# Kernel optimization log

Measured on AMD Instinct MI355X. Metric: run time of the kernel, lower is better.

Reference implementation:

```python
import jax, jax.numpy as jnp
import numpy as np

N, E, G, H, C = 50000, 800000, 512, 4, 64
DIN, DENC = 128, 256


def setup_inputs() -> dict:
    key = jax.random.key(0)
    ks = jax.random.split(key, 12)
    inp = {
        "hy": jax.random.normal(ks[0], (1, G, DENC), jnp.float32),
        "x": jax.random.normal(ks[1], (N, DIN), jnp.float32),
        "edge_index": jax.random.randint(ks[2], (2, E), 0, N, jnp.int32),
        "batch": jnp.sort(jax.random.randint(ks[3], (N,), 0, G, jnp.int32)),
        # GATv2Conv params (lin_l, lin_r: DIN -> H*C; att: [H, C]; bias: [C] since concat=False)
        "Wl": jax.random.normal(ks[4], (DIN, H * C), jnp.float32) * (1.0 / np.sqrt(DIN)),
        "bl": jnp.zeros((H * C,), jnp.float32),
        "Wr": jax.random.normal(ks[5], (DIN, H * C), jnp.float32) * (1.0 / np.sqrt(DIN)),
        "br": jnp.zeros((H * C,), jnp.float32),
        "att": jax.random.normal(ks[6], (H, C), jnp.float32) * (1.0 / np.sqrt(C)),
        "bias_gnn": jnp.zeros((C,), jnp.float32),
        # fc: (DENC + 64) -> DENC
        "Wfc": jax.random.normal(ks[7], (DENC + C, DENC), jnp.float32) * (1.0 / np.sqrt(DENC + C)),
        "bfc": jnp.zeros((DENC,), jnp.float32),
    }
    return inp


def _gatv2(x, edge_index, Wl, bl, Wr, br, att, bias_gnn):
    # add self loops (PyG default)
    loops = jnp.arange(N, dtype=edge_index.dtype)
    src = jnp.concatenate([edge_index[0], loops])
    dst = jnp.concatenate([edge_index[1], loops])
    xl = (x @ Wl + bl).reshape(N, H, C)  # source transform
    xr = (x @ Wr + br).reshape(N, H, C)  # target transform
    s = jax.nn.leaky_relu(xl[src] + xr[dst], 0.2)        # [Et, H, C]
    e = jnp.einsum('ehc,hc->eh', s, att)                 # [Et, H]
    # segment softmax over incoming edges of each dst node
    m = jax.ops.segment_max(e, dst, num_segments=N)
    m = jnp.where(jnp.isfinite(m), m, 0.0)
    a = jnp.exp(e - m[dst])
    denom = jax.ops.segment_sum(a, dst, num_segments=N)
    alpha = a / (denom[dst] + 1e-16)                     # [Et, H]
    msg = xl[src] * alpha[:, :, None]                    # [Et, H, C]
    out = jax.ops.segment_sum(msg, dst, num_segments=N)  # [N, H, C]
    return out.mean(axis=1) + bias_gnn                   # concat=False -> head mean


def reference(hy, x, edge_index, batch, Wl, bl, Wr, br, att, bias_gnn, Wfc, bfc):
    h = jax.nn.leaky_relu(_gatv2(x, edge_index, Wl, bl, Wr, br, att, bias_gnn), 0.01)
    # global mean pool per graph
    sums = jax.ops.segment_sum(h, batch, num_segments=G)
    cnts = jax.ops.segment_sum(jnp.ones((N, 1), h.dtype), batch, num_segments=G)
    hg = (sums / jnp.maximum(cnts, 1.0))[None]           # [1, G, C]
    cat = jnp.concatenate([hy, hg], axis=2)              # [1, G, DENC+C]
    return cat @ Wfc + bfc
```

## Files before the change

kernel.cpp:

```cpp
#include <hip/hip_runtime.h>

typedef unsigned short u16;
typedef __attribute__((ext_vector_type(8))) short bf16x8;
typedef __attribute__((ext_vector_type(4))) float f32x4;
typedef __attribute__((ext_vector_type(2))) float f32x2;

constexpr int N    = 50000;
constexpr int E    = 800000;
constexpr int G    = 512;
constexpr int HC   = 256;
constexpr int DIN  = 128;
constexpr int DENC = 256;
constexpr int DFC  = 320;
constexpr int NBLK = (N + 1023) / 1024;
constexpr int MT   = 64;
constexpr int XB   = (N + MT - 1) / MT;

__device__ __forceinline__ float bf2f(u16 u) {
    return __uint_as_float(((unsigned)u) << 16);
}
__device__ __forceinline__ u16 f2bf(float f) {
    unsigned u = __float_as_uint(f);
    u += 0x7fffu + ((u >> 16) & 1u);
    return (u16)(u >> 16);
}
__device__ __forceinline__ float lrelu(float v, float s) {
    return v > 0.0f ? v : v * s;
}

template<int CTRL>
__device__ __forceinline__ float dpp_radd(float x) {
    int y = __builtin_amdgcn_update_dpp(0, __float_as_int(x), CTRL, 0xF, 0xF, true);
    return x + __int_as_float(y);
}

template<bool BF> __device__ __forceinline__ float ld(const void* p, size_t i) {
    if constexpr (BF) return bf2f(((const u16*)p)[i]);
    else              return ((const float*)p)[i];
}
template<bool BF> __device__ __forceinline__ float4 ld4(const void* p, size_t i) {
    if constexpr (BF) {
        ushort4 v = ((const ushort4*)p)[i >> 2];
        return make_float4(bf2f(v.x), bf2f(v.y), bf2f(v.z), bf2f(v.w));
    } else {
        return ((const float4*)p)[i >> 2];
    }
}
template<bool BF> __device__ __forceinline__ void st(void* p, size_t i, float v) {
    if constexpr (BF) ((u16*)p)[i] = f2bf(v);
    else              ((float*)p)[i] = v;
}
__device__ __forceinline__ float ldr(const void* p, size_t i, bool bf) {
    return bf ? bf2f(((const u16*)p)[i]) : ((const float*)p)[i];
}

__global__ void k_detect(const void* x, int* flag) {
    if (blockIdx.x == 0 && threadIdx.x == 0) {
        const u16* p = (const u16*)x;
        int ok = 0;
        for (int i = 0; i < 256; i++) {
            unsigned e = (p[i] >> 7) & 0xffu;
            if (e == 0u || (e >= 100u && e <= 140u)) ok++;
        }
        *flag = (ok >= 218) ? 0 : 1;
    }
}

__global__ __launch_bounds__(64) void k_wprep(const void* Wl, const void* Wr,
                                              u16* __restrict__ whi, u16* __restrict__ wlo,
                                              const int* __restrict__ flag) {
    bool bf = (*flag == 0);
    int tile = blockIdx.x;
    int l = threadIdx.x;
    int c = tile & 31, s = tile >> 5;
    int col = c * 16 + (l & 15);
    int kbase = s * 32 + ((l >> 4) * 8);
    size_t o = (size_t)tile * 512 + (size_t)l * 8;
    #pragma unroll
    for (int j = 0; j < 8; j++) {
        int k = kbase + j;
        float v = (col < HC) ? ldr(Wl, (size_t)k * HC + col, bf)
                             : ldr(Wr, (size_t)k * HC + (col - HC), bf);
        u16 h = f2bf(v);
        whi[o + j] = h;
        wlo[o + j] = f2bf(v - bf2f(h));
    }
}

template<bool BF>
__global__ __launch_bounds__(256) void k_xlxr_t(
    const void* __restrict__ x, const u16* __restrict__ whi, const u16* __restrict__ wlo,
    const void* __restrict__ bl, const void* __restrict__ br,
    u16* __restrict__ xl, u16* __restrict__ xr, const int* __restrict__ flag) {
    if ((*flag == 0) != BF) return;
    __shared__ u16 ah[MT][136];
    __shared__ u16 al[BF ? 1 : MT][136];
    int b = blockIdx.x, t = threadIdx.x;
    int row0 = b * MT;

    {
        int k0 = (t & 15) * 8;
        #pragma unroll
        for (int it = 0; it < 4; it++) {
            int r = (t >> 4) + it * 16;
            int g = row0 + r; if (g >= N) g = N - 1;
            size_t base = (size_t)g * DIN + k0;
            if constexpr (BF) {
                const ushort4* xp = (const ushort4*)x;
                *(ushort4*)&ah[r][k0]     = xp[base >> 2];
                *(ushort4*)&ah[r][k0 + 4] = xp[(base >> 2) + 1];
            } else {
                const float4* xp = (const float4*)x;
                float4 f0 = xp[base >> 2], f1 = xp[(base >> 2) + 1];
                float v[8] = {f0.x, f0.y, f0.z, f0.w, f1.x, f1.y, f1.z, f1.w};
                #pragma unroll
                for (int j = 0; j < 8; j++) {
                    u16 h = f2bf(v[j]);
                    ah[r][k0 + j] = h;
                    al[r][k0 + j] = f2bf(v[j] - bf2f(h));
                }
            }
        }
    }
    __syncthreads();

    int w = t >> 6, l = t & 63;
    int rl = l & 15, kg = (l >> 4) * 8;
    f32x4 acc[4][8];
    #pragma unroll
    for (int rt = 0; rt < 4; rt++)
        #pragma unroll
        for (int ci = 0; ci < 8; ci++) {
            f32x4 z = {0.f, 0.f, 0.f, 0.f};
            acc[rt][ci] = z;
        }

    #pragma unroll
    for (int s = 0; s < 4; s++) {
        bf16x8 a0 = *(const bf16x8*)&ah[rl][s * 32 + kg];
        bf16x8 a1 = *(const bf16x8*)&ah[16 + rl][s * 32 + kg];
        bf16x8 a2 = *(const bf16x8*)&ah[32 + rl][s * 32 + kg];
        bf16x8 a3 = *(const bf16x8*)&ah[48 + rl][s * 32 + kg];
        #pragma unroll
        for (int ci = 0; ci < 8; ci++) {
            int c = w * 8 + ci;
            size_t fo = ((size_t)(s * 32 + c) * 64 + l) * 8;
            bf16x8 bh = *(const bf16x8*)&whi[fo];
            acc[0][ci] = __builtin_amdgcn_mfma_f32_16x16x32_bf16(a0, bh, acc[0][ci], 0, 0, 0);
            acc[1][ci] = __builtin_amdgcn_mfma_f32_16x16x32_bf16(a1, bh, acc[1][ci], 0, 0, 0);
            acc[2][ci] = __builtin_amdgcn_mfma_f32_16x16x32_bf16(a2, bh, acc[2][ci], 0, 0, 0);
            acc[3][ci] = __builtin_amdgcn_mfma_f32_16x16x32_bf16(a3, bh, acc[3][ci], 0, 0, 0);
            if constexpr (!BF) {
                bf16x8 e0 = *(const bf16x8*)&al[rl][s * 32 + kg];
                bf16x8 e1 = *(const bf16x8*)&al[16 + rl][s * 32 + kg];
                bf16x8 e2 = *(const bf16x8*)&al[32 + rl][s * 32 + kg];
                bf16x8 e3 = *(const bf16x8*)&al[48 + rl][s * 32 + kg];
                bf16x8 bw = *(const bf16x8*)&wlo[fo];
                acc[0][ci] = __builtin_amdgcn_mfma_f32_16x16x32_bf16(a0, bw, acc[0][ci], 0, 0, 0);
                acc[0][ci] = __builtin_amdgcn_mfma_f32_16x16x32_bf16(e0, bh, acc[0][ci], 0, 0, 0);
                acc[1][ci] = __builtin_amdgcn_mfma_f32_16x16x32_bf16(a1, bw, acc[1][ci], 0, 0, 0);
                acc[1][ci] = __builtin_amdgcn_mfma_f32_16x16x32_bf16(e1, bh, acc[1][ci], 0, 0, 0);
                acc[2][ci] = __builtin_amdgcn_mfma_f32_16x16x32_bf16(a2, bw, acc[2][ci], 0, 0, 0);
                acc[2][ci] = __builtin_amdgcn_mfma_f32_16x16x32_bf16(e2, bh, acc[2][ci], 0, 0, 0);
                acc[3][ci] = __builtin_amdgcn_mfma_f32_16x16x32_bf16(a3, bw, acc[3][ci], 0, 0, 0);
                acc[3][ci] = __builtin_amdgcn_mfma_f32_16x16x32_bf16(e3, bh, acc[3][ci], 0, 0, 0);
            }
        }
    }
    __syncthreads();

    float fbias[8];
    #pragma unroll
    for (int ci = 0; ci < 8; ci++) {
        int col = (w * 8 + ci) * 16 + (l & 15);
        fbias[ci] = (col < HC) ? ld<BF>(bl, col) : ld<BF>(br, col - HC);
    }

    u16 (*ep)[520] = reinterpret_cast<u16 (*)[520]>(&ah[0][0]);
    int r4 = (l >> 4) * 4;
    #pragma unroll
    for (int rt = 0; rt < 4; rt++) {
        #pragma unroll
        for (int ci = 0; ci < 8; ci++) {
            int col = (w * 8 + ci) * 16 + (l & 15);
            #pragma unroll
            for (int i = 0; i < 4; i++)
                ep[r4 + i][col] = f2bf(acc[rt][ci][i] + fbias[ci]);
        }
        __syncthreads();
        #pragma unroll
        for (int j = 0; j < 4; j++) {
            int q   = t + 256 * j;
            int row = q >> 6;
            int ck  = q & 63;
            int gr  = row0 + rt * 16 + row;
            uint4 v = *(const uint4*)&ep[row][ck * 8];
            int col0 = ck * 8;
            if (gr < N) {
                u16* dst = (col0 < HC) ? xl : xr;
                int  cc  = col0 & (HC - 1);
                *(uint4*)&dst[(size_t)gr * HC + cc] = v;
            }
        }
        __syncthreads();
    }
}

__global__ void k_deg(const int* __restrict__ ei, int* __restrict__ deg) {
    int e = blockIdx.x * blockDim.x + threadIdx.x;
    if (e < E) {
        int d = ei[E + e];
        if ((unsigned)d < (unsigned)N) atomicAdd(&deg[d], 1);
    }
}

__global__ void k_chunksum(const int* __restrict__ deg, int* __restrict__ blocksum) {
    int b = blockIdx.x, t = threadIdx.x;
    int base = b * 1024 + t * 4;
    int s = 0;
    #pragma unroll
    for (int i = 0; i < 4; i++) { int idx = base + i; if (idx < N) s += deg[idx]; }
    for (int off = 32; off; off >>= 1) s += __shfl_down(s, off, 64);
    __shared__ int ls[4];
    int wave = t >> 6;
    if ((t & 63) == 0) ls[wave] = s;
    __syncthreads();
    if (t == 0) blocksum[b] = ls[0] + ls[1] + ls[2] + ls[3];
}

__global__ void k_scanoff(int* __restrict__ blocksum, int* __restrict__ rowptr) {
    if (threadIdx.x == 0 && blockIdx.x == 0) {
        int run = 0;
        for (int b = 0; b < NBLK; b++) { int v = blocksum[b]; blocksum[b] = run; run += v; }
        rowptr[N] = run;
    }
}

__global__ void k_scanwrite(const int* __restrict__ deg, const int* __restrict__ blocksum,
                            int* __restrict__ rowptr) {
    int b = blockIdx.x, t = threadIdx.x;
    int base = b * 1024 + t * 4;
    int v[4]; int s = 0;
    #pragma unroll
    for (int i = 0; i < 4; i++) { v[i] = (base + i < N) ? deg[base + i] : 0; s += v[i]; }
    int lane = t & 63, wave = t >> 6;
    int x = s;
    for (int off = 1; off < 64; off <<= 1) {
        int y = __shfl_up(x, off, 64);
        if (lane >= off) x += y;
    }
    __shared__ int wtot[4];
    if (lane == 63) wtot[wave] = x;
    __syncthreads();
    int woff = 0;
    for (int w = 0; w < wave; w++) woff += wtot[w];
    int run = blocksum[b] + woff + (x - s);
    #pragma unroll
    for (int i = 0; i < 4; i++) {
        int idx = base + i;
        if (idx < N) rowptr[idx] = run;
        run += v[i];
    }
}

__global__ void k_fill(const int* __restrict__ ei, const int* __restrict__ rowptr,
                       int* __restrict__ cursor, int* __restrict__ col) {
    int e = blockIdx.x * blockDim.x + threadIdx.x;
    if (e < E) {
        int d = ei[E + e];
        if ((unsigned)d < (unsigned)N) {
            int pos = atomicAdd(&cursor[d], 1);
            unsigned idx = (unsigned)(rowptr[d] + pos);
            int s = ei[e];
            if (idx < (unsigned)E) col[idx] = ((unsigned)s < (unsigned)N) ? s : d;
        }
    }
}

template<bool BF>
__device__ void gat_body(const u16* __restrict__ xl, const u16* __restrict__ xr,
                         const int* __restrict__ rowptr, const int* __restrict__ col,
                         const void* __restrict__ att, const void* __restrict__ bias_gnn,
                         float* __restrict__ hnode) {
    int wid = (blockIdx.x * blockDim.x + threadIdx.x) >> 6;
    int lane = threadIdx.x & 63;
    if (wid >= N) return;
    int node = wid;

    const char* xlb = (const char*)xl;
    unsigned loff = (unsigned)lane << 3;
    auto loadrow = [&](int src) -> uint2 {
        return *(const uint2*)(xlb + (((unsigned)src << 9) + loff));
    };

    uint2 xrv = *(const uint2*)(((const char*)xr) + (((unsigned)node << 9) + loff));
    f32x2 ra, rb;
    ra.x = __uint_as_float(xrv.x << 16);
    ra.y = __uint_as_float(xrv.x & 0xffff0000u);
    rb.x = __uint_as_float(xrv.y << 16);
    rb.y = __uint_as_float(xrv.y & 0xffff0000u);
    float4 atv = ld4<BF>(att, (size_t)lane * 4);
    f32x2 ta = {atv.x, atv.y}, tb = {atv.z, atv.w};

    float l = 0.f;
    f32x2 aa = {0.f, 0.f}, ab = {0.f, 0.f};

    auto edge = [&](uint2 xv) {
        f32x2 xa, xb;
        xa.x = __uint_as_float(xv.x << 16);
        xa.y = __uint_as_float(xv.x & 0xffff0000u);
        xb.x = __uint_as_float(xv.y << 16);
        xb.y = __uint_as_float(xv.y & 0xffff0000u);
        f32x2 ua = xa + ra, ub = xb + rb;
        f32x2 sa = __builtin_elementwise_max(ua * 0.2f, ua);
        f32x2 sb = __builtin_elementwise_max(ub * 0.2f, ub);
        f32x2 d  = sa * ta + sb * tb;
        float p = d.x + d.y;
        p = dpp_radd<0xB1>(p);
        p = dpp_radd<0x4E>(p);
        p = dpp_radd<0x141>(p);
        p = dpp_radd<0x140>(p);
        float wgt = __expf(fminf(p, 80.0f));
        l += wgt;
        f32x2 wv = {wgt, wgt};
        aa = aa + xa * wv;
        ab = ab + xb * wv;
    };

    edge(loadrow(node));

    int beg = rowptr[node], end = rowptr[node + 1];
    beg = max(0, min(beg, E));
    end = max(beg, min(end, E));
    beg = __builtin_amdgcn_readfirstlane(beg);
    end = __builtin_amdgcn_readfirstlane(end);

    constexpr int UNR = 8;
    int j = beg;
    for (; j + UNR <= end; j += UNR) {
        int srcs[UNR];
        #pragma unroll
        for (int u = 0; u < UNR; u++) srcs[u] = col[j + u];
        uint2 vv[UNR];
        #pragma unroll
        for (int u = 0; u < UNR; u++) vv[u] = loadrow(srcs[u]);
        #pragma unroll
        for (int u = 0; u < UNR; u++) edge(vv[u]);
    }
    for (; j < end; j++) edge(loadrow(col[j]));

    float inv = 1.0f / (l + 1e-16f);
    float a0 = aa.x * inv, a1 = aa.y * inv, a2 = ab.x * inv, a3 = ab.y * inv;
    a0 += __shfl_xor(a0, 16); a0 += __shfl_xor(a0, 32);
    a1 += __shfl_xor(a1, 16); a1 += __shfl_xor(a1, 32);
    a2 += __shfl_xor(a2, 16); a2 += __shfl_xor(a2, 32);
    a3 += __shfl_xor(a3, 16); a3 += __shfl_xor(a3, 32);
    if (lane < 16) {
        float4 bv = ld4<BF>(bias_gnn, (size_t)lane * 4);
        float4 o;
        o.x = lrelu(a0 * 0.25f + bv.x, 0.01f);
        o.y = lrelu(a1 * 0.25f + bv.y, 0.01f);
        o.z = lrelu(a2 * 0.25f + bv.z, 0.01f);
        o.w = lrelu(a3 * 0.25f + bv.w, 0.01f);
        reinterpret_cast<float4*>(hnode)[(size_t)node * 16 + lane] = o;
    }
}

__global__ __launch_bounds__(256, 8) void k_gat(
    const u16* xl, const u16* xr, const int* rowptr, const int* col,
    const void* att, const void* bias_gnn, float* hnode, const int* flag) {
    if (*flag == 0) gat_body<true>(xl, xr, rowptr, col, att, bias_gnn, hnode);
    else            gat_body<false>(xl, xr, rowptr, col, att, bias_gnn, hnode);
}

__global__ __launch_bounds__(256) void k_pool(const float* __restrict__ hnode,
                                              const int* __restrict__ batch,
                                              float* __restrict__ hg) {
    int g = blockIdx.x, t = threadIdx.x;
    int lane = t & 63, w = t >> 6;
    int lo = 0, hi = N;
    while (lo < hi) { int mid = (lo + hi) >> 1; if (batch[mid] < g) lo = mid + 1; else hi = mid; }
    int s0 = lo;
    hi = N;
    while (lo < hi) { int mid = (lo + hi) >> 1; if (batch[mid] < g + 1) lo = mid + 1; else hi = mid; }
    int s1 = lo;
    float sum = 0.f;
    for (int n = s0 + w; n < s1; n += 4) sum += hnode[(size_t)n * 64 + lane];
    __shared__ float red[4][64];
    red[w][lane] = sum;
    __syncthreads();
    if (w == 0) {
        float s = red[0][lane] + red[1][lane] + red[2][lane] + red[3][lane];
        int cnt = s1 - s0; if (cnt < 1) cnt = 1;
        hg[g * 64 + lane] = s / (float)cnt;
    }
}

template<bool BF>
__device__ void fc_body(const void* __restrict__ hy, const float* __restrict__ hg,
                        const void* __restrict__ Wfc, const void* __restrict__ bfc,
                        void* __restrict__ out) {
    int g = blockIdx.x, t = threadIdx.x;
    __shared__ float cat[DFC];
    cat[t] = ld<BF>(hy, (size_t)g * DENC + t);
    if (t < 64) cat[DENC + t] = hg[g * 64 + t];
    __syncthreads();
    float acc = ld<BF>(bfc, t);
    for (int k = 0; k < DFC; k++) acc = fmaf(cat[k], ld<BF>(Wfc, (size_t)k * DENC + t), acc);
    st<BF>(out, (size_t)g * DENC + t, acc);
}

__global__ __launch_bounds__(256) void k_fc(
    const void* hy, const float* hg, const void* Wfc, const void* bfc,
    void* out, const int* flag) {
    if (*flag == 0) fc_body<true>(hy, hg, Wfc, bfc, out);
    else            fc_body<false>(hy, hg, Wfc, bfc, out);
}

extern "C" void kernel_launch(void* const* d_in, const int* in_sizes, int n_in,
                              void* d_out, int out_size, void* d_ws, size_t ws_size,
                              hipStream_t stream) {
    const void* hy   = d_in[0];
    const void* x    = d_in[1];
    const int*  ei   = (const int*)d_in[2];
    const int*  batch= (const int*)d_in[3];
    const void* Wl   = d_in[4];
    const void* bl   = d_in[5];
    const void* Wr   = d_in[6];
    const void* br   = d_in[7];
    const void* att  = d_in[8];
    const void* bias = d_in[9];
    const void* Wfc  = d_in[10];
    const void* bfc  = d_in[11];

    char* w = (char*)d_ws;
    u16*  xl      = (u16*)w;   w += (size_t)N * HC * 2;
    u16*  xr      = (u16*)w;   w += (size_t)N * HC * 2;
    float* hnode  = (float*)w; w += (size_t)N * 64 * 4;
    float* hg     = (float*)w; w += (size_t)G * 64 * 4;
    int*  col     = (int*)w;   w += (size_t)E * 4;
    int*  rowptr  = (int*)w;   w += ((size_t)N + 16) * 4;
    int*  blocksum= (int*)w;   w += 64 * 4;
    int*  flag    = (int*)w;   w += 64 * 4;
    int*  deg     = (int*)w;   w += (size_t)N * 4;
    int*  cursor  = (int*)w;   w += (size_t)N * 4;
    u16*  whi     = (u16*)w;   w += (size_t)4 * 32 * 64 * 8 * 2;
    u16*  wlo     = (u16*)w;   w += (size_t)4 * 32 * 64 * 8 * 2;

    hipMemsetAsync(deg, 0, (size_t)2 * N * 4, stream);

    k_detect<<<1, 64, 0, stream>>>(x, flag);
    k_wprep<<<128, 64, 0, stream>>>(Wl, Wr, whi, wlo, flag);
    k_xlxr_t<true ><<<XB, 256, 0, stream>>>(x, whi, wlo, bl, br, xl, xr, flag);
    k_xlxr_t<false><<<XB, 256, 0, stream>>>(x, whi, wlo, bl, br, xl, xr, flag);
    k_deg<<<(E + 255) / 256, 256, 0, stream>>>(ei, deg);
    k_chunksum<<<NBLK, 256, 0, stream>>>(deg, blocksum);
    k_scanoff<<<1, 64, 0, stream>>>(blocksum, rowptr);
    k_scanwrite<<<NBLK, 256, 0, stream>>>(deg, blocksum, rowptr);
    k_fill<<<(E + 255) / 256, 256, 0, stream>>>(ei, rowptr, cursor, col);
    k_gat<<<(N * 64 + 255) / 256, 256, 0, stream>>>(xl, xr, rowptr, col, att, bias, hnode, flag);
    k_pool<<<G, 256, 0, stream>>>(hnode, batch, hg);
    k_fc<<<G, 256, 0, stream>>>(hy, hg, Wfc, bfc, d_out, flag);
}
```

Measured before the change: 320.9 us.

## Split xl/xr GEMM blocks by output half to cut registers and raise occupancy

The projection kernel now launches twice as many blocks, each computing either the xl or the xr half of the 512 output columns for a 64-row tile. This halves the accumulator array per thread and merges the hi/lo LDS buffers, with launch bounds requesting four blocks per CU, so more waves can hide latency. The cost is that every x tile is loaded and split into bf16 hi/lo twice, once per column half, and the epilogue is simplified to write into a single destination.

```diff
diff --git a/kernel.cpp b/kernel.cpp
--- a/kernel.cpp
+++ b/kernel.cpp
@@ -15,6 +15,7 @@
 constexpr int NBLK = (N + 1023) / 1024;
 constexpr int MT   = 64;
 constexpr int XB   = (N + MT - 1) / MT;
+constexpr int CBLK = 4;
 
 __device__ __forceinline__ float bf2f(u16 u) {
     return __uint_as_float(((unsigned)u) << 16);
@@ -88,15 +89,15 @@
 }
 
 template<bool BF>
-__global__ __launch_bounds__(256) void k_xlxr_t(
+__global__ __launch_bounds__(256, 4) void k_xlxr_t(
     const void* __restrict__ x, const u16* __restrict__ whi, const u16* __restrict__ wlo,
     const void* __restrict__ bl, const void* __restrict__ br,
     u16* __restrict__ xl, u16* __restrict__ xr, const int* __restrict__ flag) {
     if ((*flag == 0) != BF) return;
-    __shared__ u16 ah[MT][136];
-    __shared__ u16 al[BF ? 1 : MT][136];
+    __shared__ u16 ah[(BF ? 1 : 2) * MT][136];
     int b = blockIdx.x, t = threadIdx.x;
-    int row0 = b * MT;
+    int rb = b >> 1, cg = b & 1;
+    int row0 = rb * MT;
 
     {
         int k0 = (t & 15) * 8;
@@ -117,7 +118,7 @@
                 for (int j = 0; j < 8; j++) {
                     u16 h = f2bf(v[j]);
                     ah[r][k0 + j] = h;
-                    al[r][k0 + j] = f2bf(v[j] - bf2f(h));
+                    ah[MT + r][k0 + j] = f2bf(v[j] - bf2f(h));
                 }
             }
         }
@@ -126,11 +127,11 @@
 
     int w = t >> 6, l = t & 63;
     int rl = l & 15, kg = (l >> 4) * 8;
-    f32x4 acc[4][8];
+    f32x4 acc[4][CBLK];
     #pragma unroll
     for (int rt = 0; rt < 4; rt++)
         #pragma unroll
-        for (int ci = 0; ci < 8; ci++) {
+        for (int ci = 0; ci < CBLK; ci++) {
             f32x4 z = {0.f, 0.f, 0.f, 0.f};
             acc[rt][ci] = z;
         }
@@ -142,8 +143,8 @@
         bf16x8 a2 = *(const bf16x8*)&ah[32 + rl][s * 32 + kg];
         bf16x8 a3 = *(const bf16x8*)&ah[48 + rl][s * 32 + kg];
         #pragma unroll
-        for (int ci = 0; ci < 8; ci++) {
-            int c = w * 8 + ci;
+        for (int ci = 0; ci < CBLK; ci++) {
+            int c = cg * 16 + w * CBLK + ci;
             size_t fo = ((size_t)(s * 32 + c) * 64 + l) * 8;
             bf16x8 bh = *(const bf16x8*)&whi[fo];
             acc[0][ci] = __builtin_amdgcn_mfma_f32_16x16x32_bf16(a0, bh, acc[0][ci], 0, 0, 0);
@@ -151,10 +152,10 @@
             acc[2][ci] = __builtin_amdgcn_mfma_f32_16x16x32_bf16(a2, bh, acc[2][ci], 0, 0, 0);
             acc[3][ci] = __builtin_amdgcn_mfma_f32_16x16x32_bf16(a3, bh, acc[3][ci], 0, 0, 0);
             if constexpr (!BF) {
-                bf16x8 e0 = *(const bf16x8*)&al[rl][s * 32 + kg];
-                bf16x8 e1 = *(const bf16x8*)&al[16 + rl][s * 32 + kg];
-                bf16x8 e2 = *(const bf16x8*)&al[32 + rl][s * 32 + kg];
-                bf16x8 e3 = *(const bf16x8*)&al[48 + rl][s * 32 + kg];
+                bf16x8 e0 = *(const bf16x8*)&ah[MT + rl][s * 32 + kg];
+                bf16x8 e1 = *(const bf16x8*)&ah[MT + 16 + rl][s * 32 + kg];
+                bf16x8 e2 = *(const bf16x8*)&ah[MT + 32 + rl][s * 32 + kg];
+                bf16x8 e3 = *(const bf16x8*)&ah[MT + 48 + rl][s * 32 + kg];
                 bf16x8 bw = *(const bf16x8*)&wlo[fo];
                 acc[0][ci] = __builtin_amdgcn_mfma_f32_16x16x32_bf16(a0, bw, acc[0][ci], 0, 0, 0);
                 acc[0][ci] = __builtin_amdgcn_mfma_f32_16x16x32_bf16(e0, bh, acc[0][ci], 0, 0, 0);
@@ -169,38 +170,34 @@
     }
     __syncthreads();
 
-    float fbias[8];
-    #pragma unroll
-    for (int ci = 0; ci < 8; ci++) {
-        int col = (w * 8 + ci) * 16 + (l & 15);
-        fbias[ci] = (col < HC) ? ld<BF>(bl, col) : ld<BF>(br, col - HC);
-    }
-
-    u16 (*ep)[520] = reinterpret_cast<u16 (*)[520]>(&ah[0][0]);
+    float fbias[CBLK];
+    #pragma unroll
+    for (int ci = 0; ci < CBLK; ci++) {
+        int colm = ((cg * 16 + w * CBLK + ci) * 16 + (l & 15)) & (HC - 1);
+        fbias[ci] = ld<BF>(cg ? br : bl, colm);
+    }
+    u16* dst = cg ? xr : xl;
+
+    u16 (*ep)[264] = reinterpret_cast<u16 (*)[264]>(&ah[0][0]);
     int r4 = (l >> 4) * 4;
     #pragma unroll
     for (int rt = 0; rt < 4; rt++) {
         #pragma unroll
-        for (int ci = 0; ci < 8; ci++) {
-            int col = (w * 8 + ci) * 16 + (l & 15);
+        for (int ci = 0; ci < CBLK; ci++) {
+            int colm = ((cg * 16 + w * CBLK + ci) * 16 + (l & 15)) & (HC - 1);
             #pragma unroll
             for (int i = 0; i < 4; i++)
-                ep[r4 + i][col] = f2bf(acc[rt][ci][i] + fbias[ci]);
+                ep[r4 + i][colm] = f2bf(acc[rt][ci][i] + fbias[ci]);
         }
         __syncthreads();
         #pragma unroll
-        for (int j = 0; j < 4; j++) {
+        for (int j = 0; j < 2; j++) {
             int q   = t + 256 * j;
-            int row = q >> 6;
-            int ck  = q & 63;
+            int row = q >> 5;
+            int ck  = q & 31;
             int gr  = row0 + rt * 16 + row;
             uint4 v = *(const uint4*)&ep[row][ck * 8];
-            int col0 = ck * 8;
-            if (gr < N) {
-                u16* dst = (col0 < HC) ? xl : xr;
-                int  cc  = col0 & (HC - 1);
-                *(uint4*)&dst[(size_t)gr * HC + cc] = v;
-            }
+            if (gr < N) *(uint4*)&dst[(size_t)gr * HC + ck * 8] = v;
         }
         __syncthreads();
     }
@@ -451,8 +448,8 @@
 
     k_detect<<<1, 64, 0, stream>>>(x, flag);
     k_wprep<<<128, 64, 0, stream>>>(Wl, Wr, whi, wlo, flag);
-    k_xlxr_t<true ><<<XB, 256, 0, stream>>>(x, whi, wlo, bl, br, xl, xr, flag);
-    k_xlxr_t<false><<<XB, 256, 0, stream>>>(x, whi, wlo, bl, br, xl, xr, flag);
+    k_xlxr_t<true ><<<XB * 2, 256, 0, stream>>>(x, whi, wlo, bl, br, xl, xr, flag);
+    k_xlxr_t<false><<<XB * 2, 256, 0, stream>>>(x, whi, wlo, bl, br, xl, xr, flag);
     k_deg<<<(E + 255) / 256, 256, 0, stream>>>(ei, deg);
     k_chunksum<<<NBLK, 256, 0, stream>>>(deg, blocksum);
     k_scanoff<<<1, 64, 0, stream>>>(blocksum, rowptr);
```

Measured after the change: 317.9 us. About the same (-0.9%).
